# Optimization experiments

Hardware: AMD Instinct MI355X
Metric: run time of the kernel (lower is better)

Reference implementation:

```python
import jax, jax.numpy as jnp
import numpy as np

E = 400000          # total child edges in the ready batch
P = 100000          # number of parent nodes (segments)
D = 256             # 2 * model_dim


def setup_inputs() -> dict:
    key = jax.random.key(0)
    ks = jax.random.split(key, 6)
    child_hs = jax.random.normal(ks[0], (E, D), dtype=jnp.float32)
    child_cs = jax.random.normal(ks[1], (E, D), dtype=jnp.float32)
    segment_ids = jnp.sort(jax.random.randint(ks[2], (E,), 0, P))
    W_gates = jax.random.normal(ks[3], (D, 3 * D), dtype=jnp.float32) * (1.0 / np.sqrt(D))
    b_gates = jnp.zeros((3 * D,), dtype=jnp.float32)
    W_f = jax.random.normal(ks[4], (D, D), dtype=jnp.float32) * (1.0 / np.sqrt(D))
    b_f = jnp.zeros((D,), dtype=jnp.float32)
    return {
        "child_hs": child_hs,
        "child_cs": child_cs,
        "segment_ids": segment_ids,
        "num_segments": P,
        "W_gates": W_gates,
        "b_gates": b_gates,
        "W_f": W_f,
        "b_f": b_f,
    }


def reference(child_hs, child_cs, segment_ids, num_segments, W_gates, b_gates, W_f, b_f):
    # child_hs_sum per parent (segment reduce over children)
    hs_sum = jax.ops.segment_sum(child_hs, segment_ids, num_segments=num_segments)  # [P, D]
    # gates = Linear(2*model_dim -> 6*model_dim), chunk into i, o, g
    gates = hs_sum @ W_gates + b_gates                         # [P, 3D]
    i, o, g = jnp.split(gates, 3, axis=1)
    i, o, g = jax.nn.sigmoid(i), jax.nn.sigmoid(o), jnp.tanh(g)
    # per-child forget gates, fc = f * c, segment-reduced per parent
    f = jax.nn.sigmoid(child_hs @ W_f + b_f)                   # [E, D]
    fc = jax.ops.segment_sum(f * child_cs, segment_ids, num_segments=num_segments)  # [P, D]
    # child-sum LSTM update
    c = i * g + fc
    h = o * jnp.tanh(c)
    return h, c
```

## Files before the change

kernel.cpp:

```cpp
#include <hip/hip_runtime.h>
#include <hip/hip_bf16.h>

typedef __attribute__((ext_vector_type(8))) short short8;
typedef __attribute__((ext_vector_type(4))) float floatx4;

#define DD 256

__device__ __forceinline__ unsigned short f2bf(float f) {
    unsigned int u = __builtin_bit_cast(unsigned int, f);
    u += 0x7FFFu + ((u >> 16) & 1u);
    return (unsigned short)(u >> 16);
}

__device__ __forceinline__ float sigm(float x) { return 1.0f / (1.0f + __expf(-x)); }
__device__ __forceinline__ float tanh_fast(float x) { return 2.0f / (1.0f + __expf(-2.0f * x)) - 1.0f; }

__device__ __forceinline__ short8 pack8(float4 a, float4 b) {
    short8 r;
    r[0] = (short)f2bf(a.x); r[1] = (short)f2bf(a.y);
    r[2] = (short)f2bf(a.z); r[3] = (short)f2bf(a.w);
    r[4] = (short)f2bf(b.x); r[5] = (short)f2bf(b.y);
    r[6] = (short)f2bf(b.z); r[7] = (short)f2bf(b.w);
    return r;
}

__device__ __forceinline__ void stage16(const unsigned short* g, unsigned short* l) {
    __builtin_amdgcn_global_load_lds(
        (const __attribute__((address_space(1))) unsigned int*)g,
        (__attribute__((address_space(3))) unsigned int*)l, 16, 0, 0);
}

__global__ void pack_weights(const float* __restrict__ W_f, const float* __restrict__ W_g,
                             unsigned short* __restrict__ WfT, unsigned short* __restrict__ WgT) {
    int idx = blockIdx.x * 256 + threadIdx.x;
    if (idx < 65536) {
        int n = idx >> 8, k = idx & 255;
        WfT[idx] = f2bf(W_f[k * 256 + n]);
    } else {
        int i2 = idx - 65536;
        int n = i2 >> 8, k = i2 & 255;
        WgT[i2] = f2bf(W_g[k * 768 + n]);
    }
}

__global__ void build_start(const int* __restrict__ seg, int E, int P, int* __restrict__ start) {
    int e = blockIdx.x * blockDim.x + threadIdx.x;
    if (e >= E) return;
    int s = seg[e];
    if (e == 0) {
        for (int p = 0; p <= s; ++p) start[p] = 0;
    } else {
        int sp = seg[e - 1];
        for (int p = sp + 1; p <= s; ++p) start[p] = e;
    }
    if (e == E - 1) {
        for (int p = s + 1; p <= P; ++p) start[p] = E;
    }
}

__global__ void hs_reduce(const float* __restrict__ child_hs, const int* __restrict__ start,
                          int P, float* __restrict__ hs_sum) {
    int wave = threadIdx.x >> 6, lane = threadIdx.x & 63;
    int p = blockIdx.x * 4 + wave;
    if (p >= P) return;
    int lo = start[p], hi = start[p + 1];
    float4 acc = make_float4(0.f, 0.f, 0.f, 0.f);
    const float4* src = (const float4*)child_hs;
    for (int e = lo; e < hi; ++e) {
        float4 v = src[(size_t)e * 64 + lane];
        acc.x += v.x; acc.y += v.y; acc.z += v.z; acc.w += v.w;
    }
    ((float4*)hs_sum)[(size_t)p * 64 + lane] = acc;
}

__global__ __launch_bounds__(256, 2) void gemm1_fc(
    const float* __restrict__ child_hs, const float* __restrict__ child_cs,
    const int* __restrict__ seg, const unsigned short* __restrict__ WfT,
    const float* __restrict__ b_f, float* __restrict__ fc, int E) {
    __shared__ __align__(16) unsigned short ldsB[2][8192];
    const int tid = threadIdx.x;
    const int w = tid >> 6, lane = tid & 63;
    const int nl = lane & 15, q = lane >> 4;
    const int e_base = blockIdx.x * 64 + w * 16;

    floatx4 acc[16];
#pragma unroll
    for (int t = 0; t < 16; ++t) acc[t] = (floatx4){0.f, 0.f, 0.f, 0.f};

    const float* Arow = child_hs + (size_t)(e_base + nl) * DD + q * 8;
    const unsigned short* Wsrc = WfT + ((w * 64 + nl) << 8) + q * 8;

#pragma unroll
    for (int r = 0; r < 4; ++r)
        stage16(Wsrc + (r << 12), &ldsB[0][(w * 4 + r) << 9]);
    float4 a0 = *(const float4*)(Arow);
    float4 a1 = *(const float4*)(Arow + 4);
    short8 af = pack8(a0, a1);
    __syncthreads();

    for (int ks = 0; ks < 8; ++ks) {
        const unsigned short* lcur = ldsB[ks & 1];
        float4 b0, b1;
        if (ks < 7) {
            unsigned short* lnxt = ldsB[(ks + 1) & 1];
            const unsigned short* ws = Wsrc + (ks + 1) * 32;
#pragma unroll
            for (int r = 0; r < 4; ++r)
                stage16(ws + (r << 12), &lnxt[(w * 4 + r) << 9]);
            b0 = *(const float4*)(Arow + (ks + 1) * 32);
            b1 = *(const float4*)(Arow + (ks + 1) * 32 + 4);
        }
#pragma unroll
        for (int t = 0; t < 16; ++t) {
            short8 bf = ((const short8*)lcur)[t * 64 + lane];
            acc[t] = __builtin_amdgcn_mfma_f32_16x16x32_bf16(af, bf, acc[t], 0, 0, 0);
        }
        if (ks < 7) af = pack8(b0, b1);
        __syncthreads();
    }

    int e0 = e_base + q * 4;
    int s0 = seg[e0], s1 = seg[e0 + 1], s2 = seg[e0 + 2], s3 = seg[e0 + 3];
#pragma unroll
    for (int t = 0; t < 16; ++t) {
        int n = t * 16 + nl;
        float bias = b_f[n];
        float v0 = sigm(acc[t][0] + bias) * child_cs[(size_t)(e0 + 0) * DD + n];
        float v1 = sigm(acc[t][1] + bias) * child_cs[(size_t)(e0 + 1) * DD + n];
        float v2 = sigm(acc[t][2] + bias) * child_cs[(size_t)(e0 + 2) * DD + n];
        float v3 = sigm(acc[t][3] + bias) * child_cs[(size_t)(e0 + 3) * DD + n];
        float a = v0; int s = s0;
        if (s1 == s) { a += v1; } else { atomicAdd(&fc[(size_t)s * DD + n], a); a = v1; s = s1; }
        if (s2 == s) { a += v2; } else { atomicAdd(&fc[(size_t)s * DD + n], a); a = v2; s = s2; }
        if (s3 == s) { a += v3; } else { atomicAdd(&fc[(size_t)s * DD + n], a); a = v3; s = s3; }
        atomicAdd(&fc[(size_t)s * DD + n], a);
    }
}

__global__ __launch_bounds__(512, 2) void gemm2_lstm(
    const float* __restrict__ hs_sum, const unsigned short* __restrict__ WgT,
    const float* __restrict__ b_g, float* __restrict__ h_out, float* __restrict__ c_out, int P) {
    __shared__ __align__(16) unsigned short ldsB[24576];
    const int tid = threadIdx.x;
    const int w = tid >> 6, lane = tid & 63;
    const int wr = w >> 2, wc = w & 3;
    const int nl = lane & 15, q = lane >> 4;
    const int p_base = blockIdx.x * 64;

    floatx4 acc[2][12];
#pragma unroll
    for (int rt = 0; rt < 2; ++rt)
#pragma unroll
        for (int t = 0; t < 12; ++t) acc[rt][t] = (floatx4){0.f, 0.f, 0.f, 0.f};

    const float* Arow0 = hs_sum + (size_t)(p_base + wr * 32 + nl) * DD + q * 8;
    const float* Arow1 = Arow0 + (size_t)16 * DD;
    const unsigned short* Wsrc = WgT + ((w * 96 + nl) << 8) + q * 8;

#pragma unroll
    for (int r = 0; r < 6; ++r)
        stage16(Wsrc + (r << 12), &ldsB[(w * 6 + r) << 9]);

    for (int ks = 0; ks < 8; ++ks) {
        float4 a0 = *(const float4*)(Arow0 + ks * 32);
        float4 a1 = *(const float4*)(Arow0 + ks * 32 + 4);
        float4 a2 = *(const float4*)(Arow1 + ks * 32);
        float4 a3 = *(const float4*)(Arow1 + ks * 32 + 4);
        short8 af0 = pack8(a0, a1);
        short8 af1 = pack8(a2, a3);
        __syncthreads();
#pragma unroll
        for (int cgl = 0; cgl < 4; ++cgl) {
#pragma unroll
            for (int part = 0; part < 3; ++part) {
                int t = part * 16 + (wc * 4 + cgl);
                short8 bf = ((const short8*)ldsB)[t * 64 + lane];
                acc[0][cgl * 3 + part] =
                    __builtin_amdgcn_mfma_f32_16x16x32_bf16(af0, bf, acc[0][cgl * 3 + part], 0, 0, 0);
                acc[1][cgl * 3 + part] =
                    __builtin_amdgcn_mfma_f32_16x16x32_bf16(af1, bf, acc[1][cgl * 3 + part], 0, 0, 0);
            }
        }
        __syncthreads();
        if (ks < 7) {
            const unsigned short* ws = Wsrc + (ks + 1) * 32;
#pragma unroll
            for (int r = 0; r < 6; ++r)
                stage16(ws + (r << 12), &ldsB[(w * 6 + r) << 9]);
        }
    }

#pragma unroll
    for (int rt = 0; rt < 2; ++rt) {
#pragma unroll
        for (int cgl = 0; cgl < 4; ++cgl) {
            int n = (wc * 4 + cgl) * 16 + nl;
            float bi = b_g[n], bo = b_g[256 + n], bg = b_g[512 + n];
#pragma unroll
            for (int reg = 0; reg < 4; ++reg) {
                int p = p_base + wr * 32 + rt * 16 + q * 4 + reg;
                if (p < P) {
                    float I = acc[rt][cgl * 3 + 0][reg] + bi;
                    float O = acc[rt][cgl * 3 + 1][reg] + bo;
                    float G = acc[rt][cgl * 3 + 2][reg] + bg;
                    float iv = sigm(I), ov = sigm(O), gv = tanh_fast(G);
                    float c = iv * gv + c_out[(size_t)p * DD + n];
                    float hv = ov * tanh_fast(c);
                    h_out[(size_t)p * DD + n] = hv;
                    c_out[(size_t)p * DD + n] = c;
                }
            }
        }
    }
}

extern "C" void kernel_launch(void* const* d_in, const int* in_sizes, int n_in,
                              void* d_out, int out_size, void* d_ws, size_t ws_size,
                              hipStream_t stream) {
    const float* child_hs = (const float*)d_in[0];
    const float* child_cs = (const float*)d_in[1];
    const int*   seg      = (const int*)d_in[2];
    const float* W_gates  = (const float*)d_in[4];
    const float* b_gates  = (const float*)d_in[5];
    const float* W_f      = (const float*)d_in[6];
    const float* b_f      = (const float*)d_in[7];

    const int D = 256;
    const int E = in_sizes[0] / D;
    const int P = out_size / (2 * D);

    float* h_out = (float*)d_out;
    float* c_out = (float*)d_out + (size_t)P * D;

    unsigned short* WfT = (unsigned short*)d_ws;
    unsigned short* WgT = WfT + 65536;
    int* start = (int*)(WgT + 196608);

    hipMemsetAsync(c_out, 0, (size_t)P * D * sizeof(float), stream);

    pack_weights<<<1024, 256, 0, stream>>>(W_f, W_gates, WfT, WgT);
    build_start<<<(E + 255) / 256, 256, 0, stream>>>(seg, E, P, start);
    hs_reduce<<<(P + 3) / 4, 256, 0, stream>>>(child_hs, start, P, h_out);
    gemm1_fc<<<E / 64, 256, 0, stream>>>(child_hs, child_cs, seg, WfT, b_f, c_out, E);
    gemm2_lstm<<<(P + 63) / 64, 512, 0, stream>>>(h_out, WgT, b_gates, h_out, c_out, P);
}
```

Baseline: 1.401 ms.

## Assign parent segments to blocks and reduce forget-gate products in LDS

gemm1_fc now gives each block a range of 32 parents and loops over their child edges in 64-row chunks. The per-child f*c products are accumulated with LDS atomics into a shared tile, which is then written to the output once with plain stores. This removes global atomics and the memset of c_out. In exchange the K-loop loses its double-buffered weight staging and gains an extra barrier per step, and the grid uses P/32 blocks with uneven work per block. hs_reduce is also unrolled by four for more loads in flight, and the P/32 grid would leave tail parents uncomputed if P were not a multiple of 32.

```diff
diff --git a/kernel.cpp b/kernel.cpp
--- a/kernel.cpp
+++ b/kernel.cpp
@@ -5,6 +5,8 @@
 typedef __attribute__((ext_vector_type(4))) float floatx4;
 
 #define DD 256
+#define PPB 32
+#define FSTRIDE 264
 
 __device__ __forceinline__ unsigned short f2bf(float f) {
     unsigned int u = __builtin_bit_cast(unsigned int, f);
@@ -66,7 +68,18 @@
     int lo = start[p], hi = start[p + 1];
     float4 acc = make_float4(0.f, 0.f, 0.f, 0.f);
     const float4* src = (const float4*)child_hs;
-    for (int e = lo; e < hi; ++e) {
+    int e = lo;
+    for (; e + 4 <= hi; e += 4) {
+        float4 v0 = src[(size_t)(e + 0) * 64 + lane];
+        float4 v1 = src[(size_t)(e + 1) * 64 + lane];
+        float4 v2 = src[(size_t)(e + 2) * 64 + lane];
+        float4 v3 = src[(size_t)(e + 3) * 64 + lane];
+        acc.x += v0.x + v1.x + v2.x + v3.x;
+        acc.y += v0.y + v1.y + v2.y + v3.y;
+        acc.z += v0.z + v1.z + v2.z + v3.z;
+        acc.w += v0.w + v1.w + v2.w + v3.w;
+    }
+    for (; e < hi; ++e) {
         float4 v = src[(size_t)e * 64 + lane];
         acc.x += v.x; acc.y += v.y; acc.z += v.z; acc.w += v.w;
     }
@@ -75,65 +88,81 @@
 
 __global__ __launch_bounds__(256, 2) void gemm1_fc(
     const float* __restrict__ child_hs, const float* __restrict__ child_cs,
-    const int* __restrict__ seg, const unsigned short* __restrict__ WfT,
-    const float* __restrict__ b_f, float* __restrict__ fc, int E) {
-    __shared__ __align__(16) unsigned short ldsB[2][8192];
+    const int* __restrict__ seg, const int* __restrict__ start,
+    const unsigned short* __restrict__ WfT, const float* __restrict__ b_f,
+    float* __restrict__ fc, int E, int P) {
+    __shared__ __align__(16) unsigned short ldsB[8192];
+    __shared__ __align__(16) float fcacc[PPB * FSTRIDE];
     const int tid = threadIdx.x;
     const int w = tid >> 6, lane = tid & 63;
     const int nl = lane & 15, q = lane >> 4;
-    const int e_base = blockIdx.x * 64 + w * 16;
-
-    floatx4 acc[16];
-#pragma unroll
-    for (int t = 0; t < 16; ++t) acc[t] = (floatx4){0.f, 0.f, 0.f, 0.f};
-
-    const float* Arow = child_hs + (size_t)(e_base + nl) * DD + q * 8;
+    const int p0 = blockIdx.x * PPB;
+    const int lo = start[p0], hi = start[p0 + PPB];
+
+    for (int i = tid; i < PPB * FSTRIDE / 4; i += 256)
+        ((float4*)fcacc)[i] = make_float4(0.f, 0.f, 0.f, 0.f);
+
     const unsigned short* Wsrc = WfT + ((w * 64 + nl) << 8) + q * 8;
 
-#pragma unroll
-    for (int r = 0; r < 4; ++r)
-        stage16(Wsrc + (r << 12), &ldsB[0][(w * 4 + r) << 9]);
-    float4 a0 = *(const float4*)(Arow);
-    float4 a1 = *(const float4*)(Arow + 4);
-    short8 af = pack8(a0, a1);
+    for (int cb = lo; cb < hi; cb += 64) {
+        floatx4 acc[16];
+#pragma unroll
+        for (int t = 0; t < 16; ++t) acc[t] = (floatx4){0.f, 0.f, 0.f, 0.f};
+
+        int erow = cb + w * 16 + nl;
+        const float* Arow = child_hs + (size_t)(erow < E ? erow : E - 1) * DD + q * 8;
+
+        for (int ks = 0; ks < 8; ++ks) {
+            __syncthreads();
+#pragma unroll
+            for (int r = 0; r < 4; ++r)
+                stage16(Wsrc + ks * 32 + (r << 12), &ldsB[(w * 4 + r) << 9]);
+            float4 a0 = *(const float4*)(Arow + ks * 32);
+            float4 a1 = *(const float4*)(Arow + ks * 32 + 4);
+            short8 af = pack8(a0, a1);
+            __syncthreads();
+#pragma unroll
+            for (int t = 0; t < 16; ++t) {
+                short8 bf = ((const short8*)ldsB)[t * 64 + lane];
+                acc[t] = __builtin_amdgcn_mfma_f32_16x16x32_bf16(af, bf, acc[t], 0, 0, 0);
+            }
+        }
+
+        int e0 = cb + w * 16 + q * 4;
+        int sr[4];
+#pragma unroll
+        for (int r = 0; r < 4; ++r) {
+            int e = e0 + r;
+            sr[r] = (e < hi) ? (seg[e] - p0) : -1;
+        }
+#pragma unroll
+        for (int t = 0; t < 16; ++t) {
+            int n = t * 16 + nl;
+            float bias = b_f[n];
+            float vr[4];
+#pragma unroll
+            for (int r = 0; r < 4; ++r) {
+                float cs = (sr[r] >= 0) ? child_cs[(size_t)(e0 + r) * DD + n] : 0.f;
+                vr[r] = sigm(acc[t][r] + bias) * cs;
+            }
+            float a = vr[0]; int s = sr[0];
+#pragma unroll
+            for (int r = 1; r < 4; ++r) {
+                if (sr[r] == s) { a += vr[r]; }
+                else {
+                    if (s >= 0) atomicAdd(&fcacc[s * FSTRIDE + n], a);
+                    a = vr[r]; s = sr[r];
+                }
+            }
+            if (s >= 0) atomicAdd(&fcacc[s * FSTRIDE + n], a);
+        }
+    }
+
     __syncthreads();
-
-    for (int ks = 0; ks < 8; ++ks) {
-        const unsigned short* lcur = ldsB[ks & 1];
-        float4 b0, b1;
-        if (ks < 7) {
-            unsigned short* lnxt = ldsB[(ks + 1) & 1];
-            const unsigned short* ws = Wsrc + (ks + 1) * 32;
-#pragma unroll
-            for (int r = 0; r < 4; ++r)
-                stage16(ws + (r << 12), &lnxt[(w * 4 + r) << 9]);
-            b0 = *(const float4*)(Arow + (ks + 1) * 32);
-            b1 = *(const float4*)(Arow + (ks + 1) * 32 + 4);
-        }
-#pragma unroll
-        for (int t = 0; t < 16; ++t) {
-            short8 bf = ((const short8*)lcur)[t * 64 + lane];
-            acc[t] = __builtin_amdgcn_mfma_f32_16x16x32_bf16(af, bf, acc[t], 0, 0, 0);
-        }
-        if (ks < 7) af = pack8(b0, b1);
-        __syncthreads();
-    }
-
-    int e0 = e_base + q * 4;
-    int s0 = seg[e0], s1 = seg[e0 + 1], s2 = seg[e0 + 2], s3 = seg[e0 + 3];
-#pragma unroll
-    for (int t = 0; t < 16; ++t) {
-        int n = t * 16 + nl;
-        float bias = b_f[n];
-        float v0 = sigm(acc[t][0] + bias) * child_cs[(size_t)(e0 + 0) * DD + n];
-        float v1 = sigm(acc[t][1] + bias) * child_cs[(size_t)(e0 + 1) * DD + n];
-        float v2 = sigm(acc[t][2] + bias) * child_cs[(size_t)(e0 + 2) * DD + n];
-        float v3 = sigm(acc[t][3] + bias) * child_cs[(size_t)(e0 + 3) * DD + n];
-        float a = v0; int s = s0;
-        if (s1 == s) { a += v1; } else { atomicAdd(&fc[(size_t)s * DD + n], a); a = v1; s = s1; }
-        if (s2 == s) { a += v2; } else { atomicAdd(&fc[(size_t)s * DD + n], a); a = v2; s = s2; }
-        if (s3 == s) { a += v3; } else { atomicAdd(&fc[(size_t)s * DD + n], a); a = v3; s = s3; }
-        atomicAdd(&fc[(size_t)s * DD + n], a);
+    for (int i = tid; i < PPB * 64; i += 256) {
+        int row = i >> 6, c4 = i & 63;
+        float4 v = *(const float4*)&fcacc[row * FSTRIDE + c4 * 4];
+        ((float4*)fc)[(((size_t)(p0 + row)) << 6) + c4] = v;
     }
 }
 
@@ -236,11 +265,9 @@
     unsigned short* WgT = WfT + 65536;
     int* start = (int*)(WgT + 196608);
 
-    hipMemsetAsync(c_out, 0, (size_t)P * D * sizeof(float), stream);
-
     pack_weights<<<1024, 256, 0, stream>>>(W_f, W_gates, WfT, WgT);
     build_start<<<(E + 255) / 256, 256, 0, stream>>>(seg, E, P, start);
     hs_reduce<<<(P + 3) / 4, 256, 0, stream>>>(child_hs, start, P, h_out);
-    gemm1_fc<<<E / 64, 256, 0, stream>>>(child_hs, child_cs, seg, WfT, b_f, c_out, E);
+    gemm1_fc<<<P / PPB, 256, 0, stream>>>(child_hs, child_cs, seg, start, WfT, b_f, c_out, E, P);
     gemm2_lstm<<<(P + 63) / 64, 512, 0, stream>>>(h_out, WgT, b_gates, h_out, c_out, P);
 }
```

Result: slower. 1.483 ms (+5.9%).
